# Optimization experiments

Measured on AMD Instinct MI355X. Metric: run time of the kernel, lower is better.

## Reference

```python
import jax, jax.numpy as jnp
import numpy as np

D_MODEL = 1024
NUM_HEADS = 16
DK = D_MODEL // NUM_HEADS
THETA = 10000.0
B, S = 4, 2048


def _rope(x, pos):
    # x: [B, H, S, dk], pos: [S] int positions
    half = DK // 2
    inv_freq = THETA ** (-jnp.arange(half, dtype=jnp.float32) * 2.0 / DK)  # [half]
    ang = pos.astype(jnp.float32)[:, None] * inv_freq[None, :]             # [S, half]
    cos, sin = jnp.cos(ang), jnp.sin(ang)                                  # [S, half]
    x_even = x[..., 0::2]
    x_odd = x[..., 1::2]
    out_even = x_even * cos - x_odd * sin
    out_odd = x_even * sin + x_odd * cos
    # interleave back to [..., dk]
    return jnp.stack([out_even, out_odd], axis=-1).reshape(x.shape)


def setup_inputs() -> dict:
    key = jax.random.key(0)
    ks = jax.random.split(key, 5)
    scale = 1.0 / np.sqrt(D_MODEL)
    return {
        "x": jax.random.normal(ks[0], (B, S, D_MODEL), dtype=jnp.float32),
        "token_position": jnp.arange(S, dtype=jnp.int32),
        "wq": jax.random.normal(ks[1], (D_MODEL, D_MODEL), dtype=jnp.float32) * scale,
        "wk": jax.random.normal(ks[2], (D_MODEL, D_MODEL), dtype=jnp.float32) * scale,
        "wv": jax.random.normal(ks[3], (D_MODEL, D_MODEL), dtype=jnp.float32) * scale,
        "wo": jax.random.normal(ks[4], (D_MODEL, D_MODEL), dtype=jnp.float32) * scale,
    }


def reference(x, token_position, wq, wk, wv, wo):
    b, s, _ = x.shape
    # QKV projections (torch Linear: y = x @ W.T), split heads -> [B, H, S, dk]
    def proj(w):
        y = jnp.einsum("bsd,ed->bse", x, w)
        return y.reshape(b, s, NUM_HEADS, DK).transpose(0, 2, 1, 3)
    q, k, v = proj(wq), proj(wk), proj(wv)
    q = _rope(q, token_position)
    k = _rope(k, token_position)
    # causal SDPA
    scores = jnp.einsum("bhqd,bhkd->bhqk", q, k) / jnp.sqrt(jnp.float32(DK))
    causal = jnp.tril(jnp.ones((s, s), dtype=bool))
    scores = jnp.where(causal, scores, -jnp.inf)
    attn = jax.nn.softmax(scores, axis=-1)
    out = jnp.einsum("bhqk,bhkd->bhqd", attn, v)          # [B, H, S, dv]
    out = out.transpose(0, 2, 1, 3).reshape(b, s, D_MODEL)  # merge heads
    return jnp.einsum("bsd,ed->bse", out, wo)             # output projection
```

## Files before the change

### kernel.cpp

```cpp
#include <hip/hip_runtime.h>


#define D_MODEL 1024
#define NH      16
#define DKH     64
#define SEQ     2048
#define BATCH   4
#define SCALE_LOG2 0.180336875461f
#define ROPE_L2    0.41524101186092029f

typedef _Float16 f16;
typedef _Float16 f16x8 __attribute__((ext_vector_type(8)));
typedef _Float16 f16x4 __attribute__((ext_vector_type(4)));
typedef __fp16   fp16x2n __attribute__((ext_vector_type(2)));
typedef float    f32x4 __attribute__((ext_vector_type(4)));
typedef unsigned short u16;
typedef unsigned int   u32;

__device__ __forceinline__ void glds16(const void* g, void* l) {
  __builtin_amdgcn_global_load_lds((const __attribute__((address_space(1))) void*)g,
                                   (__attribute__((address_space(3))) void*)l, 16, 0, 0);
}
__device__ __forceinline__ u32 pk(float a, float b) {
  union { fp16x2n h; u32 u; } c; c.h = __builtin_amdgcn_cvt_pkrtz(a, b); return c.u;
}

#define VMW_(N) asm volatile("s_waitcnt vmcnt(" #N ")" ::: "memory")
#define VMW(N) VMW_(N)
#define BAR() __builtin_amdgcn_s_barrier()

__global__ void cvt_all(const float* __restrict__ x,
                        const float* __restrict__ w0, const float* __restrict__ w1,
                        const float* __restrict__ w2, const float* __restrict__ w3,
                        f16* __restrict__ xo, f16* __restrict__ o0, f16* __restrict__ o1,
                        f16* __restrict__ o2, f16* __restrict__ o3) {
  int blk = blockIdx.x;
  const float* src; f16* dst; int off;
  if (blk < 8192) { src = x; dst = xo; off = blk; }
  else {
    int t = blk - 8192; int w = t >> 10; off = t & 1023;
    switch (w) { case 0: src = w0; dst = o0; break;  case 1: src = w1; dst = o1; break;
                 case 2: src = w2; dst = o2; break;  default: src = w3; dst = o3; break; }
  }
  int i = (off * 256 + threadIdx.x) * 4;
  float4 v = *(const float4*)(src + i);
  uint2 o; o.x = pk(v.x, v.y); o.y = pk(v.z, v.w);
  *(uint2*)(dst + i) = o;
}

__global__ __launch_bounds__(512, 2) void gemm_qkv(const f16* __restrict__ A,
                                                   const f16* __restrict__ W,
                                                   f16* __restrict__ Qo,
                                                   f16* __restrict__ Ko,
                                                   f16* __restrict__ Vo,
                                                   const int* __restrict__ pos) {
  extern __shared__ char lds[];
  const int bid  = blockIdx.x;
  const int lin  = (bid & 7) * 64 + (bid >> 3);
  const int bx   = lin & 15, by = lin >> 4;
  const int m0   = by * 256, n0 = bx * 192;
  const int tid  = threadIdx.x;
  const int wave = tid >> 6, lane = tid & 63;
  const int quad = lane >> 4, l16 = lane & 15;
  const int wr   = wave >> 2, wc = wave & 3;

  f32x4 acc[8][3];
#pragma unroll
  for (int i = 0; i < 8; ++i)
#pragma unroll
    for (int j = 0; j < 3; ++j) acc[i][j] = (f32x4){0.f, 0.f, 0.f, 0.f};

  const int posR = (l16 & 1) * 4 + (quad ^ ((l16 >> 1) & 3));
  const char* aRd  = lds + wr * 8192 + (l16 >> 1) * 128 + posR * 16;
  const char* bRd0 = lds + 65536 + (wc * 48 + l16) * 128 + ((quad) ^ (l16 & 7)) * 16;
  const char* bRd1 = lds + 65536 + (wc * 48 + l16) * 128 + ((4 + quad) ^ (l16 & 7)) * 16;

  const int srA = tid >> 3;
  const int rA  = 2 * srA + ((tid >> 2) & 1);
  const int cA  = (tid & 3) ^ (srA & 3);
  const f16* pA0 = A + (size_t)(m0 + rA) * 1024 + cA * 8;
  const f16* pA1 = pA0 + (size_t)128 * 1024;
  const int gB = (tid & 7) ^ ((tid >> 3) & 7);
  const f16* pB0 = W + (size_t)(n0 + (tid >> 3)) * 1024 + gB * 8;
  const f16* pB1 = pB0 + (size_t)64 * 1024;
  const f16* pB2 = pB0 + (size_t)128 * 1024;
  char* const sdA = lds + (size_t)(tid & 448) * 16;
  char* const sdB = lds + 65536 + (size_t)(tid & 448) * 16;

#define ST_A(TB, H) do {                                                      \
    glds16(pA0 + (H) * 32, sdA + (TB) * 32768 + (H) * 16384);                 \
    glds16(pA1 + (H) * 32, sdA + (TB) * 32768 + (H) * 16384 + 8192);          \
  } while (0)
#define ST_B(TB) do {                                                         \
    glds16(pB0, sdB + (TB) * 24576);                                          \
    glds16(pB1, sdB + (TB) * 24576 + 8192);                                   \
    glds16(pB2, sdB + (TB) * 24576 + 16384);                                  \
  } while (0)
#define RDA(BUF, H, MG) do { _Pragma("unroll")                                \
    for (int i_ = 0; i_ < 4; ++i_)                                            \
      af[i_] = *(const f16x8*)(aRd + (BUF) * 32768 + (H) * 16384 +            \
                               (MG) * 4096 + i_ * 1024);                      \
  } while (0)
#define RDB(BUF, H) do { _Pragma("unroll")                                    \
    for (int j_ = 0; j_ < 3; ++j_)                                            \
      bf[j_] = *(const f16x8*)(((H) ? bRd1 : bRd0) + (BUF) * 24576 + j_ * 2048);\
  } while (0)
#define MMQ(MG) do {                                                          \
    __builtin_amdgcn_s_setprio(1);                                            \
    _Pragma("unroll")                                                         \
    for (int i_ = 0; i_ < 4; ++i_) { _Pragma("unroll")                        \
      for (int j_ = 0; j_ < 3; ++j_)                                          \
        acc[(MG) * 4 + i_][j_] = __builtin_amdgcn_mfma_f32_16x16x32_f16(      \
            af[i_], bf[j_], acc[(MG) * 4 + i_][j_], 0, 0, 0); }               \
    __builtin_amdgcn_s_setprio(0);                                            \
  } while (0)

#define TILE(BUF, DOSTAGE, VM2, LAST) do {                                    \
    f16x8 af[4]; f16x8 bf[3];                                                 \
    RDA(BUF, 0, 0); RDB(BUF, 0);                                              \
    if (DOSTAGE) ST_A((BUF) ^ 1, 0);                                          \
    BAR(); MMQ(0);                                                            \
    BAR();                                                                    \
    RDA(BUF, 0, 1);                                                           \
    if (DOSTAGE) ST_B((BUF) ^ 1);                                             \
    BAR(); MMQ(1);                                                            \
    VMW(VM2);                                                                 \
    BAR();                                                                    \
    RDA(BUF, 1, 0); RDB(BUF, 1);                                              \
    if (DOSTAGE) ST_A((BUF) ^ 1, 1);                                          \
    BAR(); MMQ(0);                                                            \
    BAR();                                                                    \
    RDA(BUF, 1, 1);                                                           \
    BAR(); MMQ(1);                                                            \
    if (!(LAST)) {                                                            \
      VMW_(2);                                                                \
      BAR();                                                                  \
    }                                                                         \
    if (DOSTAGE) { pA0 += 64; pA1 += 64; pB0 += 64; pB1 += 64; pB2 += 64; }   \
  } while (0)

  ST_A(0, 0); ST_B(0); ST_A(0, 1);
  pA0 += 64; pA1 += 64; pB0 += 64; pB1 += 64; pB2 += 64;
  VMW_(2);
  BAR();

#pragma unroll 1
  for (int it = 0; it < 7; ++it) {
    TILE(0, 1, 5, 0);
    TILE(1, 1, 5, 0);
  }
  TILE(0, 1, 5, 0);
  TILE(1, 0, 0, 1);

#undef TILE
#undef MMQ
#undef RDB
#undef RDA
#undef ST_B
#undef ST_A

  f16* dsts[3]; int colB[3]; bool rp[3]; float invf[3], sgn[3];
#pragma unroll
  for (int ni = 0; ni < 3; ++ni) {
    int gc  = n0 + wc * 48 + ni * 16 + l16;
    int seg = gc >> 10;
    dsts[ni] = (seg == 0) ? Qo : (seg == 1) ? Ko : Vo;
    colB[ni] = gc & 1023;
    rp[ni]   = (seg < 2);
    int dk   = gc & 63;
    invf[ni] = __builtin_amdgcn_exp2f(-ROPE_L2 * (float)(dk >> 1));
    sgn[ni]  = (dk & 1) ? 1.f : -1.f;
  }
#pragma unroll
  for (int a = 0; a < 8; ++a)
#pragma unroll
    for (int r = 0; r < 4; ++r) {
      int row = m0 + wr * 128 + a * 16 + quad * 4 + r;
      float ps = (float)pos[row & (SEQ - 1)];
#pragma unroll
      for (int ni = 0; ni < 3; ++ni) {
        float v = acc[a][ni][r];
        float ov;
        if (rp[ni]) {
          float ang = ps * invf[ni];
          float c = __cosf(ang), sn = __sinf(ang);
          float p = __shfl_xor(v, 1);
          ov = fmaf(p * sgn[ni], sn, v * c);
        } else ov = v;
        dsts[ni][(size_t)row * 1024 + colB[ni]] = (f16)ov;
      }
    }
}

__global__ __launch_bounds__(512, 2) void gemm_out(const f16* __restrict__ A,
                                                   const f16* __restrict__ W,
                                                   float* __restrict__ C) {
  extern __shared__ char lds[];
  const int bid  = blockIdx.x;
  const int lin  = (bid & 7) * 32 + (bid >> 3);
  const int bx   = lin & 3, by = lin >> 2;
  const int m0   = by * 128, n0 = bx * 256;
  const int tid  = threadIdx.x;
  const int wave = tid >> 6, lane = tid & 63;
  const int quad = lane >> 4, l16 = lane & 15;
  const int wr   = wave >> 2, wc = wave & 3;

  f32x4 acc[4][4];
#pragma unroll
  for (int i = 0; i < 4; ++i)
#pragma unroll
    for (int j = 0; j < 4; ++j) acc[i][j] = (f32x4){0.f, 0.f, 0.f, 0.f};

  const int posR = (l16 & 1) * 4 + (quad ^ ((l16 >> 1) & 3));
  const char* aRd = lds + wr * 4096 + (l16 >> 1) * 128 + posR * 16;
  const char* bRd = lds + 32768 + wc * 4096 + (l16 >> 1) * 128 + posR * 16;

  const int srA = tid >> 3;
  const int rA  = 2 * srA + ((tid >> 2) & 1);
  const int cA  = (tid & 3) ^ (srA & 3);
  const f16* pA = A + (size_t)(m0 + rA) * 1024 + cA * 8;
  const int rB  = 2 * (tid >> 3) + ((tid >> 2) & 1);
  const int cB  = (tid & 3) ^ ((tid >> 3) & 3);
  const f16* pB0 = W + (size_t)(n0 + rB) * 1024 + cB * 8;
  const f16* pB1 = pB0 + (size_t)128 * 1024;
  char* const sdA = lds + (size_t)(tid & 448) * 16;
  char* const sdB = lds + 32768 + (size_t)(tid & 448) * 16;

#define ST_AO(TB, H) glds16(pA + (H) * 32, sdA + (TB) * 16384 + (H) * 8192)
#define ST_BO(TB, H) do {                                                     \
    glds16(pB0 + (H) * 32, sdB + (TB) * 32768 + (H) * 16384);                 \
    glds16(pB1 + (H) * 32, sdB + (TB) * 32768 + (H) * 16384 + 8192);          \
  } while (0)
#define HALF(BUF, H, DOSTAGE, VMN, LAST) do {                                 \
    f16x8 af[4], bf[4];                                                       \
    _Pragma("unroll")                                                         \
    for (int i_ = 0; i_ < 4; ++i_)                                            \
      af[i_] = *(const f16x8*)(aRd + (BUF) * 16384 + (H) * 8192 + i_ * 1024); \
    _Pragma("unroll")                                                         \
    for (int j_ = 0; j_ < 4; ++j_)                                            \
      bf[j_] = *(const f16x8*)(bRd + (BUF) * 32768 + (H) * 16384 + j_ * 1024);\
    if (DOSTAGE) { ST_AO((BUF) ^ 1, H); ST_BO((BUF) ^ 1, H); }                \
    BAR();                                                                    \
    __builtin_amdgcn_s_setprio(1);                                            \
    _Pragma("unroll")                                                         \
    for (int i_ = 0; i_ < 4; ++i_) { _Pragma("unroll")                        \
      for (int j_ = 0; j_ < 4; ++j_)                                          \
        acc[i_][j_] = __builtin_amdgcn_mfma_f32_16x16x32_f16(                 \
            af[i_], bf[j_], acc[i_][j_], 0, 0, 0); }                          \
    __builtin_amdgcn_s_setprio(0);                                            \
    if (!(LAST)) {                                                            \
      VMW(VMN);                                                               \
      BAR();                                                                  \
    }                                                                         \
  } while (0)

  ST_AO(0, 0); ST_BO(0, 0); ST_AO(0, 1); ST_BO(0, 1);
  pA += 64; pB0 += 64; pB1 += 64;
  VMW_(3);
  BAR();

#pragma unroll 1
  for (int it = 0; it < 7; ++it) {
    HALF(0, 0, 1, 3, 0); HALF(0, 1, 1, 3, 0); pA += 64; pB0 += 64; pB1 += 64;
    HALF(1, 0, 1, 3, 0); HALF(1, 1, 1, 3, 0); pA += 64; pB0 += 64; pB1 += 64;
  }
  HALF(0, 0, 1, 3, 0); HALF(0, 1, 1, 3, 0);
  HALF(1, 0, 0, 0, 0);
  HALF(1, 1, 0, 0, 1);

#undef HALF
#undef ST_BO
#undef ST_AO

  float* dst = C;
#pragma unroll
  for (int a = 0; a < 4; ++a)
#pragma unroll
    for (int ni = 0; ni < 4; ++ni)
#pragma unroll
      for (int r = 0; r < 4; ++r) {
        int row = m0 + wr * 64 + a * 16 + quad * 4 + r;
        int col = n0 + wc * 64 + ni * 16 + l16;
        dst[(size_t)row * 1024 + col] = acc[a][ni][r];
      }
}

__global__ __launch_bounds__(256, 3) void flash_attn(const f16* __restrict__ Q,
                                                     const f16* __restrict__ Kg,
                                                     const f16* __restrict__ Vg,
                                                     f16* __restrict__ O) {
  __shared__ char smem[38400];
  f16*  KsL         = (f16*)smem;
  u32   (*Vt)[67]   = (u32(*)[67])(smem + 16384);
  float (*Red0)[66] = (float(*)[66])smem;
  float (*Red1)[66] = (float(*)[66])(smem + 16896);
  float (*Lb)[17]   = (float(*)[17])(smem + 33792);

  const int tid  = threadIdx.x;
  const int bh   = blockIdx.x;
  const int b    = bh >> 4, h = bh & 15;
  const int qblk = 31 - (int)blockIdx.y;
  const int q0   = qblk * 64;
  const int wave = tid >> 6, lane = tid & 63;
  const int quad = lane >> 4, l16 = lane & 15;
  const int nkt  = (qblk + 2) >> 1;

  f16x8 qf[4][2];
#pragma unroll
  for (int nt = 0; nt < 4; ++nt)
#pragma unroll
    for (int ks = 0; ks < 2; ++ks) {
      f16x8 qv = *(const f16x8*)(Q + ((size_t)(b * SEQ + q0 + nt * 16 + l16)) * D_MODEL
                                   + h * DKH + ks * 32 + quad * 8);
      qf[nt][ks] = qv * (f16)SCALE_LOG2;
    }

  f32x4 o[4][4];
#pragma unroll
  for (int md = 0; md < 4; ++md)
#pragma unroll
    for (int nt = 0; nt < 4; ++nt) o[md][nt] = (f32x4){0.f, 0.f, 0.f, 0.f};
  float lacc[4] = {0.f, 0.f, 0.f, 0.f};

  const int kp = tid >> 3, dc = (tid & 7) * 8;

  for (int t = 0; t < nkt; ++t) {
    const int kt = t * 128;
    const f16* vb = Vg + ((size_t)(b * SEQ + kt + 2 * kp)) * D_MODEL + h * DKH + dc;
    uint4 v0 = *(const uint4*)vb;
    uint4 v1 = *(const uint4*)(vb + D_MODEL);
    uint4 v2 = *(const uint4*)(vb + 64 * D_MODEL);
    uint4 v3 = *(const uint4*)(vb + 65 * D_MODEL);

    if (t) __syncthreads();
#pragma unroll
    for (int i = 0; i < 4; ++i) {
      int ci = i * 256 + tid;
      int row = ci >> 3, gc = (ci & 7) ^ (row & 7);
      glds16(Kg + ((size_t)(b * SEQ + kt + row)) * D_MODEL + h * DKH + gc * 8,
             smem + (size_t)(i * 256 + (tid & 192)) * 16);
    }
    {
      union { uint4 u; u16 s[8]; } a0, a1, a2, a3;
      a0.u = v0; a1.u = v1; a2.u = v2; a3.u = v3;
#pragma unroll
      for (int j = 0; j < 8; ++j) {
        Vt[dc + j][kp]      = (u32)a0.s[j] | ((u32)a1.s[j] << 16);
        Vt[dc + j][32 + kp] = (u32)a2.s[j] | ((u32)a3.s[j] << 16);
      }
    }
    __syncthreads();

    f16x4 pb[2][4];
#pragma unroll
    for (int mt = 0; mt < 2; ++mt) {
      const int krow = wave * 32 + mt * 16 + l16;
      const int s0 = quad ^ (krow & 7);
      f16x8 ka0 = *(const f16x8*)(KsL + krow * 64 + s0 * 8);
      f16x8 ka1 = *(const f16x8*)(KsL + krow * 64 + (s0 ^ 4) * 8);
      const int keyb = kt + wave * 32 + mt * 16 + quad * 4;
#pragma unroll
      for (int nt = 0; nt < 4; ++nt) {
        f32x4 c = (f32x4){0.f, 0.f, 0.f, 0.f};
        c = __builtin_amdgcn_mfma_f32_16x16x32_f16(ka0, qf[nt][0], c, 0, 0, 0);
        c = __builtin_amdgcn_mfma_f32_16x16x32_f16(ka1, qf[nt][1], c, 0, 0, 0);
        const int q = q0 + nt * 16 + l16;
        float p0 = __builtin_amdgcn_exp2f(c[0]);
        float p1 = __builtin_amdgcn_exp2f(c[1]);
        float p2 = __builtin_amdgcn_exp2f(c[2]);
        float p3 = __builtin_amdgcn_exp2f(c[3]);
        if (t == nkt - 1) {
          p0 = (keyb + 0 <= q) ? p0 : 0.f;
          p1 = (keyb + 1 <= q) ? p1 : 0.f;
          p2 = (keyb + 2 <= q) ? p2 : 0.f;
          p3 = (keyb + 3 <= q) ? p3 : 0.f;
        }
        lacc[nt] += (p0 + p1) + (p2 + p3);
        union { u32 w[2]; f16x4 v; } pp;
        pp.w[0] = pk(p0, p1); pp.w[1] = pk(p2, p3);
        pb[mt][nt] = pp.v;
      }
    }

#pragma unroll
    for (int md = 0; md < 4; ++md)
#pragma unroll
      for (int ks2 = 0; ks2 < 2; ++ks2) {
        const u32* vp = &Vt[md * 16 + l16][wave * 16 + ks2 * 8 + quad * 2];
        union { u32 x[2]; f16x4 v; } va;
        va.x[0] = vp[0]; va.x[1] = vp[1];
#pragma unroll
        for (int nt = 0; nt < 4; ++nt)
          o[md][nt] = __builtin_amdgcn_mfma_f32_16x16x16f16(va.v, pb[ks2][nt], o[md][nt], 0, 0, 0);
      }
  }

  __syncthreads();
  {
    float (*Rw)[66] = (wave >= 2) ? Red1 : Red0;
    if ((wave & 1) == 0) {
#pragma unroll
      for (int md = 0; md < 4; ++md)
#pragma unroll
        for (int nt = 0; nt < 4; ++nt)
#pragma unroll
          for (int r = 0; r < 4; ++r)
            Rw[md * 16 + quad * 4 + r][nt * 16 + l16] = o[md][nt][r];
    }
#pragma unroll
    for (int nt = 0; nt < 4; ++nt)
      Lb[nt * 16 + l16][wave * 4 + quad] = lacc[nt];
    __syncthreads();
    if (wave & 1) {
#pragma unroll
      for (int md = 0; md < 4; ++md)
#pragma unroll
        for (int nt = 0; nt < 4; ++nt)
#pragma unroll
          for (int r = 0; r < 4; ++r)
            Rw[md * 16 + quad * 4 + r][nt * 16 + l16] += o[md][nt][r];
    }
    __syncthreads();
  }

  {
    const int q = tid & 63, dc4 = (tid >> 6) * 16;
    float lsum = 0.f;
#pragma unroll
    for (int j = 0; j < 16; ++j) lsum += Lb[q][j];
    float linv = __builtin_amdgcn_rcpf(lsum);
    union { uint4 u[2]; u32 w[8]; } ov;
#pragma unroll
    for (int i = 0; i < 8; ++i) {
      float f0 = Red0[dc4 + 2 * i][q]     + Red1[dc4 + 2 * i][q];
      float f1 = Red0[dc4 + 2 * i + 1][q] + Red1[dc4 + 2 * i + 1][q];
      ov.w[i] = pk(f0 * linv, f1 * linv);
    }
    f16* op = O + ((size_t)(b * SEQ + q0 + q)) * D_MODEL + h * DKH + dc4;
    *(uint4*)op = ov.u[0];
    *(uint4*)(op + 8) = ov.u[1];
  }
}

extern "C" void kernel_launch(void* const* d_in, const int* in_sizes, int n_in,
                              void* d_out, int out_size, void* d_ws, size_t ws_size,
                              hipStream_t stream) {
  const float* x      = (const float*)d_in[0];
  const int*   tokpos = (const int*)d_in[1];
  const float* wq     = (const float*)d_in[2];
  const float* wk     = (const float*)d_in[3];
  const float* wv     = (const float*)d_in[4];
  const float* wo     = (const float*)d_in[5];
  float* out = (float*)d_out;

  char* ws = (char*)d_ws;
  f16* Xb  = (f16*)(ws + 0);
  f16* Wqb = (f16*)(ws + 16777216);
  f16* Wkb = (f16*)(ws + 18874368);
  f16* Wvb = (f16*)(ws + 20971520);
  f16* Wob = (f16*)(ws + 23068672);
  f16* Qb  = (f16*)(ws + 25165824);
  f16* Kb  = (f16*)(ws + 41943040);
  f16* Vb  = (f16*)(ws + 58720256);
  f16* Ob  = Xb;

  static bool attr_done = false;
  if (!attr_done) {
    (void)hipFuncSetAttribute(reinterpret_cast<const void*>(gemm_qkv),
                              hipFuncAttributeMaxDynamicSharedMemorySize, 114688);
    (void)hipFuncSetAttribute(reinterpret_cast<const void*>(gemm_out),
                              hipFuncAttributeMaxDynamicSharedMemorySize, 98304);
    attr_done = true;
  }

  cvt_all<<<12288, 256, 0, stream>>>(x, wq, wk, wv, wo, Xb, Wqb, Wkb, Wvb, Wob);

  gemm_qkv<<<512, 512, 114688, stream>>>(Xb, Wqb, Qb, Kb, Vb, tokpos);

  flash_attn<<<dim3(BATCH * NH, 32), 256, 0, stream>>>(Qb, Kb, Vb, Ob);

  gemm_out<<<256, 512, 98304, stream>>>(Ob, Wob, out);
}
```

Baseline: 256.0 us.

## Double-buffer LDS fragment registers to overlap reads with MFMA in GEMMs

Restructures the QKV-projection and output-projection GEMM main loops so the LDS fragment reads for the next sub-step go into a second register set while MFMAs run on the current set. Several barriers are removed, and the prefetch of the next tile's first fragments crosses tile boundaries. In the output GEMM, global-to-LDS staging is regrouped so each stage covers one K-half ahead. The aim is to hide LDS latency and cut barrier stalls, at the cost of more VGPRs and tighter reliance on correct wait counts and buffer reuse.

```diff
diff --git a/kernel.cpp b/kernel.cpp
--- a/kernel.cpp
+++ b/kernel.cpp
@@ -87,6 +87,9 @@
   char* const sdA = lds + (size_t)(tid & 448) * 16;
   char* const sdB = lds + 65536 + (size_t)(tid & 448) * 16;
 
+  f16x8 af[2][4];
+  f16x8 bf[2][3];
+
 #define ST_A(TB, H) do {                                                      \
     glds16(pA0 + (H) * 32, sdA + (TB) * 32768 + (H) * 16384);                 \
     glds16(pA1 + (H) * 32, sdA + (TB) * 32768 + (H) * 16384 + 8192);          \
@@ -96,66 +99,71 @@
     glds16(pB1, sdB + (TB) * 24576 + 8192);                                   \
     glds16(pB2, sdB + (TB) * 24576 + 16384);                                  \
   } while (0)
-#define RDA(BUF, H, MG) do { _Pragma("unroll")                                \
+#define RDAF(S, BUF, H, MG) do { _Pragma("unroll")                            \
     for (int i_ = 0; i_ < 4; ++i_)                                            \
-      af[i_] = *(const f16x8*)(aRd + (BUF) * 32768 + (H) * 16384 +            \
-                               (MG) * 4096 + i_ * 1024);                      \
-  } while (0)
-#define RDB(BUF, H) do { _Pragma("unroll")                                    \
+      af[S][i_] = *(const f16x8*)(aRd + (BUF) * 32768 + (H) * 16384 +         \
+                                  (MG) * 4096 + i_ * 1024);                   \
+  } while (0)
+#define RDBF(S, BUF, H) do { _Pragma("unroll")                                \
     for (int j_ = 0; j_ < 3; ++j_)                                            \
-      bf[j_] = *(const f16x8*)(((H) ? bRd1 : bRd0) + (BUF) * 24576 + j_ * 2048);\
-  } while (0)
-#define MMQ(MG) do {                                                          \
+      bf[S][j_] = *(const f16x8*)(((H) ? bRd1 : bRd0) + (BUF) * 24576 +       \
+                                  j_ * 2048);                                 \
+  } while (0)
+#define MMQ(AS, BS, MG) do {                                                  \
     __builtin_amdgcn_s_setprio(1);                                            \
     _Pragma("unroll")                                                         \
     for (int i_ = 0; i_ < 4; ++i_) { _Pragma("unroll")                        \
       for (int j_ = 0; j_ < 3; ++j_)                                          \
         acc[(MG) * 4 + i_][j_] = __builtin_amdgcn_mfma_f32_16x16x32_f16(      \
-            af[i_], bf[j_], acc[(MG) * 4 + i_][j_], 0, 0, 0); }               \
+            af[AS][i_], bf[BS][j_], acc[(MG) * 4 + i_][j_], 0, 0, 0); }       \
     __builtin_amdgcn_s_setprio(0);                                            \
   } while (0)
 
-#define TILE(BUF, DOSTAGE, VM2, LAST) do {                                    \
-    f16x8 af[4]; f16x8 bf[3];                                                 \
-    RDA(BUF, 0, 0); RDB(BUF, 0);                                              \
-    if (DOSTAGE) ST_A((BUF) ^ 1, 0);                                          \
-    BAR(); MMQ(0);                                                            \
+#define TILEQ(BUF, DS, V1, V3) do {                                           \
+    RDAF(1, BUF, 0, 1);                                                       \
+    if (DS) ST_A((BUF) ^ 1, 0);                                               \
+    MMQ(0, 0, 0);                                                             \
+    VMW(V1); BAR();                                                           \
+    RDAF(0, BUF, 1, 0); RDBF(1, BUF, 1);                                      \
+    if (DS) ST_B((BUF) ^ 1);                                                  \
+    MMQ(1, 0, 1);                                                             \
     BAR();                                                                    \
-    RDA(BUF, 0, 1);                                                           \
-    if (DOSTAGE) ST_B((BUF) ^ 1);                                             \
-    BAR(); MMQ(1);                                                            \
-    VMW(VM2);                                                                 \
-    BAR();                                                                    \
-    RDA(BUF, 1, 0); RDB(BUF, 1);                                              \
-    if (DOSTAGE) ST_A((BUF) ^ 1, 1);                                          \
-    BAR(); MMQ(0);                                                            \
-    BAR();                                                                    \
-    RDA(BUF, 1, 1);                                                           \
-    BAR(); MMQ(1);                                                            \
-    if (!(LAST)) {                                                            \
-      VMW_(2);                                                                \
-      BAR();                                                                  \
-    }                                                                         \
-    if (DOSTAGE) { pA0 += 64; pA1 += 64; pB0 += 64; pB1 += 64; pB2 += 64; }   \
+    RDAF(1, BUF, 1, 1);                                                       \
+    if (DS) ST_A((BUF) ^ 1, 1);                                               \
+    MMQ(0, 1, 0);                                                             \
+    VMW(V3); BAR();                                                           \
+    RDAF(0, (BUF) ^ 1, 0, 0); RDBF(0, (BUF) ^ 1, 0);                          \
+    MMQ(1, 1, 1);                                                             \
+    if (DS) { pA0 += 64; pA1 += 64; pB0 += 64; pB1 += 64; pB2 += 64; }        \
   } while (0)
 
   ST_A(0, 0); ST_B(0); ST_A(0, 1);
   pA0 += 64; pA1 += 64; pB0 += 64; pB1 += 64; pB2 += 64;
   VMW_(2);
   BAR();
+  RDAF(0, 0, 0, 0);
+  RDBF(0, 0, 0);
 
 #pragma unroll 1
   for (int it = 0; it < 7; ++it) {
-    TILE(0, 1, 5, 0);
-    TILE(1, 1, 5, 0);
-  }
-  TILE(0, 1, 5, 0);
-  TILE(1, 0, 0, 1);
-
-#undef TILE
+    TILEQ(0, 1, 2, 2);
+    TILEQ(1, 1, 2, 2);
+  }
+  TILEQ(0, 1, 2, 2);
+
+  RDAF(1, 1, 0, 1);
+  MMQ(0, 0, 0);
+  VMW_(0); BAR();
+  RDAF(0, 1, 1, 0); RDBF(1, 1, 1);
+  MMQ(1, 0, 1);
+  RDAF(1, 1, 1, 1);
+  MMQ(0, 1, 0);
+  MMQ(1, 1, 1);
+
+#undef TILEQ
 #undef MMQ
-#undef RDB
-#undef RDA
+#undef RDBF
+#undef RDAF
 #undef ST_B
 #undef ST_A
 
@@ -226,51 +234,84 @@
   char* const sdA = lds + (size_t)(tid & 448) * 16;
   char* const sdB = lds + 32768 + (size_t)(tid & 448) * 16;
 
-#define ST_AO(TB, H) glds16(pA + (H) * 32, sdA + (TB) * 16384 + (H) * 8192)
-#define ST_BO(TB, H) do {                                                     \
-    glds16(pB0 + (H) * 32, sdB + (TB) * 32768 + (H) * 16384);                 \
-    glds16(pB1 + (H) * 32, sdB + (TB) * 32768 + (H) * 16384 + 8192);          \
-  } while (0)
-#define HALF(BUF, H, DOSTAGE, VMN, LAST) do {                                 \
-    f16x8 af[4], bf[4];                                                       \
-    _Pragma("unroll")                                                         \
-    for (int i_ = 0; i_ < 4; ++i_)                                            \
-      af[i_] = *(const f16x8*)(aRd + (BUF) * 16384 + (H) * 8192 + i_ * 1024); \
-    _Pragma("unroll")                                                         \
-    for (int j_ = 0; j_ < 4; ++j_)                                            \
-      bf[j_] = *(const f16x8*)(bRd + (BUF) * 32768 + (H) * 16384 + j_ * 1024);\
-    if (DOSTAGE) { ST_AO((BUF) ^ 1, H); ST_BO((BUF) ^ 1, H); }                \
-    BAR();                                                                    \
+  f16x8 oa[2][4], ob[2][4];
+
+#define ST_G1(TB) do {                                                        \
+    glds16(pA + 32,  sdA + (TB) * 16384 + 8192);                              \
+    glds16(pB0 + 32, sdB + (TB) * 32768 + 16384);                             \
+    glds16(pB1 + 32, sdB + (TB) * 32768 + 16384 + 8192);                      \
+  } while (0)
+#define ST_G0(TB) do {                                                        \
+    glds16(pA + 64,  sdA + (TB) * 16384);                                     \
+    glds16(pB0 + 64, sdB + (TB) * 32768);                                     \
+    glds16(pB1 + 64, sdB + (TB) * 32768 + 8192);                              \
+  } while (0)
+#define RDO(S, BUF, H) do { _Pragma("unroll")                                 \
+    for (int i_ = 0; i_ < 4; ++i_) {                                          \
+      oa[S][i_] = *(const f16x8*)(aRd + (BUF) * 16384 + (H) * 8192 +          \
+                                  i_ * 1024);                                 \
+      ob[S][i_] = *(const f16x8*)(bRd + (BUF) * 32768 + (H) * 16384 +         \
+                                  i_ * 1024); }                               \
+  } while (0)
+#define MMO(S) do {                                                           \
     __builtin_amdgcn_s_setprio(1);                                            \
     _Pragma("unroll")                                                         \
     for (int i_ = 0; i_ < 4; ++i_) { _Pragma("unroll")                        \
       for (int j_ = 0; j_ < 4; ++j_)                                          \
         acc[i_][j_] = __builtin_amdgcn_mfma_f32_16x16x32_f16(                 \
-            af[i_], bf[j_], acc[i_][j_], 0, 0, 0); }                          \
+            oa[S][i_], ob[S][j_], acc[i_][j_], 0, 0, 0); }                    \
     __builtin_amdgcn_s_setprio(0);                                            \
-    if (!(LAST)) {                                                            \
-      VMW(VMN);                                                               \
-      BAR();                                                                  \
-    }                                                                         \
-  } while (0)
-
-  ST_AO(0, 0); ST_BO(0, 0); ST_AO(0, 1); ST_BO(0, 1);
+  } while (0)
+
+#define OT(BUF) do {                                                          \
+    RDO(1, BUF, 1);                                               \
+    ST_G1((BUF) ^ 1);                                        \
+    MMO(0);                                                                   \
+    VMW_(3); BAR();                                                           \
+    RDO(0, (BUF) ^ 1, 0);                                       \
+    ST_G0(BUF);                                              \
+    MMO(1);                                                                   \
+    VMW_(3); BAR();                                                           \
+    pA += 64; pB0 += 64; pB1 += 64;                                           \
+  } while (0)
+
+  {
+    glds16(pA,       sdA);
+    glds16(pB0,      sdB);
+    glds16(pB1,      sdB + 8192);
+    glds16(pA + 32,  sdA + 8192);
+    glds16(pB0 + 32, sdB + 16384);
+    glds16(pB1 + 32, sdB + 16384 + 8192);
+    glds16(pA + 64,  sdA + 16384);
+    glds16(pB0 + 64, sdB + 32768);
+    glds16(pB1 + 64, sdB + 32768 + 8192);
+  }
   pA += 64; pB0 += 64; pB1 += 64;
   VMW_(3);
   BAR();
+  RDO(0, 0, 0);
 
 #pragma unroll 1
   for (int it = 0; it < 7; ++it) {
-    HALF(0, 0, 1, 3, 0); HALF(0, 1, 1, 3, 0); pA += 64; pB0 += 64; pB1 += 64;
-    HALF(1, 0, 1, 3, 0); HALF(1, 1, 1, 3, 0); pA += 64; pB0 += 64; pB1 += 64;
-  }
-  HALF(0, 0, 1, 3, 0); HALF(0, 1, 1, 3, 0);
-  HALF(1, 0, 0, 0, 0);
-  HALF(1, 1, 0, 0, 1);
-
-#undef HALF
-#undef ST_BO
-#undef ST_AO
+    OT(0);
+    OT(1);
+  }
+  RDO(1, 0, 1);
+  ST_G1(1);
+  MMO(0);
+  VMW_(3); BAR();
+  RDO(0, 1, 0);
+  MMO(1);
+  VMW_(0); BAR();
+  RDO(1, 1, 1);
+  MMO(0);
+  MMO(1);
+
+#undef OT
+#undef MMO
+#undef RDO
+#undef ST_G0
+#undef ST_G1
 
   float* dst = C;
 #pragma unroll
```

Measured after the change: 258.5 us. No clear change (+1.0%).
